# Optimization experiments

Measured on AMD Instinct MI355X. Metric: run time of the kernel, lower is better.

The kernel has to match this reference:

```python
import jax, jax.numpy as jnp
import numpy as np
from jax import lax

B, N, NPOINT, NSAMPLE = 8, 8192, 1024, 32
IN_CH = 64
MLP = [128, 128, 256]
EPS = 1e-5  # BatchNorm eps (inference mode with running stats)


def setup_inputs() -> dict:
    key = jax.random.key(0)
    ks = jax.random.split(key, 2 + len(MLP))
    inp = {
        "xyz": jax.random.normal(ks[0], (B, N, 3), jnp.float32),
        "feature": jax.random.normal(ks[1], (B, IN_CH, N), jnp.float32),
    }
    last = IN_CH
    for li, out in enumerate(MLP):
        k = jax.random.split(ks[2 + li], 3)
        inp[f"w{li}"] = jax.random.normal(k[0], (out, last), jnp.float32) / np.sqrt(last).astype(np.float32)
        inp[f"b{li}"] = jnp.zeros((out,), jnp.float32)
        inp[f"gamma{li}"] = jnp.ones((out,), jnp.float32)
        inp[f"beta{li}"] = jnp.zeros((out,), jnp.float32)
        inp[f"mean{li}"] = 0.1 * jax.random.normal(k[1], (out,), jnp.float32)
        inp[f"var{li}"] = 1.0 + 0.1 * jax.random.uniform(k[2], (out,), jnp.float32)
        last = out
    return inp


def furthest_point_sample(xyz, npoint):
    # xyz: [B, N, 3] -> idx [B, npoint] (sequential FPS via scan)
    Bn, Nn, _ = xyz.shape
    start = jnp.zeros((Bn,), jnp.int32)

    def step(carry, _):
        mind, last = carry
        p = jnp.take_along_axis(xyz, last[:, None, None], axis=1)  # [B,1,3]
        d = jnp.sum((xyz - p) ** 2, axis=-1)  # [B,N]
        mind = jnp.minimum(mind, d)
        nxt = jnp.argmax(mind, axis=-1).astype(jnp.int32)
        return (mind, nxt), nxt

    init = (jnp.full((Bn, Nn), 1e10, xyz.dtype), start)
    _, rest = lax.scan(step, init, None, length=npoint - 1)  # [npoint-1, B]
    return jnp.concatenate([start[None, :], rest], axis=0).T  # [B, npoint]


def k_neighbor_query(new_xyz, xyz, k):
    # squared distances via ||a||^2 + ||b||^2 - 2 a.b  (no [B,S,N,3] blowup)
    d = (jnp.sum(new_xyz ** 2, -1)[:, :, None]
         + jnp.sum(xyz ** 2, -1)[:, None, :]
         - 2.0 * jnp.einsum('bsc,bnc->bsn', new_xyz, xyz))  # [B,S,N]
    _, idx = lax.top_k(-d, k)  # k smallest distances
    return idx  # [B,S,k]


def _mlp_layers(x, params):
    # x: [B, Cin, S, k]; each layer: 1x1 conv -> BN (running stats) -> ReLU
    for (w, b, g, bt, m, v) in params:
        y = jnp.einsum('oi,bisk->bosk', w, x) + b[None, :, None, None]
        inv = (g / jnp.sqrt(v + EPS))[None, :, None, None]
        x = jax.nn.relu((y - m[None, :, None, None]) * inv + bt[None, :, None, None])
    return x


def reference(xyz, feature,
              w0, b0, gamma0, beta0, mean0, var0,
              w1, b1, gamma1, beta1, mean1, var1,
              w2, b2, gamma2, beta2, mean2, var2):
    idx = furthest_point_sample(xyz, NPOINT)                     # [B,S]
    new_xyz = jnp.take_along_axis(xyz, idx[:, :, None], axis=1)  # [B,S,3]
    nidx = k_neighbor_query(new_xyz, xyz, NSAMPLE)               # [B,S,k]
    # grouping_operation: gather neighbor features -> [B,D,S,k]
    grouped = jax.vmap(lambda f, i: f[:, i])(feature, nidx)
    params = [(w0, b0, gamma0, beta0, mean0, var0),
              (w1, b1, gamma1, beta1, mean1, var1),
              (w2, b2, gamma2, beta2, mean2, var2)]
    x = _mlp_layers(grouped, params)
    new_feature = jnp.max(x, axis=3)  # [B, D', S]
    return new_xyz, new_feature
```

## Files before the change

kernel.cpp:

```cpp
#include <hip/hip_runtime.h>
#include <hip/hip_bf16.h>
#include <math.h>

#define B_  8
#define N_  8192
#define S_  1024
#define K_  32
#define C0_ 64
#define NW  248
#define BINS 2048
#define CCAP 256

typedef __attribute__((ext_vector_type(8))) short short8;
typedef __attribute__((ext_vector_type(4))) float f32x4;
typedef __attribute__((ext_vector_type(2))) float f32x2;

#define WH_OFF   0
#define WL_OFF   114688
#define SC_OFF   229376
#define SH_OFF   231424
#define FT_OFF   233472
#define NIDX_OFF 8622080
#define PROG_OFF 9670656
#define WL0E 0
#define WL1E 8192
#define WL2E 24576

__device__ __forceinline__ void split_bf16(float x, unsigned short& h, unsigned short& l) {
    __hip_bfloat16 hb = __float2bfloat16(x);
    float hf = __bfloat162float(hb);
    __hip_bfloat16 lb = __float2bfloat16(x - hf);
    h = *(unsigned short*)&hb;
    l = *(unsigned short*)&lb;
}

__device__ __forceinline__ f32x4 mfma16(short8 a, short8 b, f32x4 c) {
    return __builtin_amdgcn_mfma_f32_16x16x32_bf16(a, b, c, 0, 0, 0);
}

template<int CTRL, int RMASK>
__device__ __forceinline__ unsigned long long dpp_max_step(unsigned long long k) {
    unsigned lo = (unsigned)k, hi = (unsigned)(k >> 32);
    unsigned tlo = (unsigned)__builtin_amdgcn_update_dpp(0, (int)lo, CTRL, RMASK, 0xF, false);
    unsigned thi = (unsigned)__builtin_amdgcn_update_dpp(0, (int)hi, CTRL, RMASK, 0xF, false);
    unsigned long long t = ((unsigned long long)thi << 32) | (unsigned long long)tlo;
    return (t > k) ? t : k;
}
__device__ __forceinline__ unsigned long long wave_max_u64(unsigned long long k) {
    k = dpp_max_step<0x111, 0xF>(k);
    k = dpp_max_step<0x112, 0xF>(k);
    k = dpp_max_step<0x114, 0xF>(k);
    k = dpp_max_step<0x118, 0xF>(k);
    k = dpp_max_step<0x142, 0xA>(k);
    k = dpp_max_step<0x143, 0xC>(k);
    return k;
}
__device__ __forceinline__ unsigned long long umax64(unsigned long long a, unsigned long long b) {
    return (a > b) ? a : b;
}

struct KnnSh {
    unsigned hist[2][BINS];
    unsigned long long cand[2][CCAP];
    unsigned long long kslots[2][2][4];
    int sel[2][K_];
    unsigned wpart[2][4];
    int sBin[2], sBelow[2];
    unsigned cnt_sel[2], cnt_cand[2];
    int fallback;
};

__global__ __launch_bounds__(512) void fused_kernel(
    const float* __restrict__ xyz, const float* __restrict__ feature,
    const float* __restrict__ w0, const float* __restrict__ w1, const float* __restrict__ w2,
    const float* __restrict__ b0, const float* __restrict__ g0, const float* __restrict__ be0,
    const float* __restrict__ m0, const float* __restrict__ v0,
    const float* __restrict__ b1, const float* __restrict__ g1, const float* __restrict__ be1,
    const float* __restrict__ m1, const float* __restrict__ v1,
    const float* __restrict__ b2, const float* __restrict__ g2, const float* __restrict__ be2,
    const float* __restrict__ m2, const float* __restrict__ v2,
    char* __restrict__ ws, float* __restrict__ out)
{
    __shared__ __align__(16) char smraw[131584];
    const int tid = threadIdx.x;
    const int bid = (int)blockIdx.x;

    if (bid < B_) {
        #pragma clang fp contract(off)
        const int b = bid;
        float4* xyzw = (float4*)smraw;
        unsigned long long* wredA = (unsigned long long*)(smraw + N_ * 16);
        unsigned long long* wredB = wredA + 8;
        int* prog = (int*)(ws + PROG_OFF) + b * 16;

        f32x2 px[8], py[8], pz[8], mind[8];
        const float* xb = xyz + (size_t)b * N_ * 3;
        #pragma unroll
        for (int j = 0; j < 8; ++j) {
            int n0 = (2 * j) * 512 + tid, n1 = n0 + 512;
            float x0 = xb[n0 * 3], y0 = xb[n0 * 3 + 1], z0 = xb[n0 * 3 + 2];
            float x1 = xb[n1 * 3], y1 = xb[n1 * 3 + 1], z1 = xb[n1 * 3 + 2];
            px[j] = (f32x2){x0, x1}; py[j] = (f32x2){y0, y1}; pz[j] = (f32x2){z0, z1};
            xyzw[n0] = make_float4(x0, y0, z0, 0.f);
            xyzw[n1] = make_float4(x1, y1, z1, 0.f);
            mind[j] = (f32x2){1e10f, 1e10f};
        }
        __syncthreads();

        float4 p0 = xyzw[0];
        float lx = p0.x, ly = p0.y, lz = p0.z;
        if (tid == 0) {
            float* d0 = out + (size_t)b * S_ * 3;
            d0[0] = lx; d0[1] = ly; d0[2] = lz;
        }
        const int lane = tid & 63, wid = tid >> 6;

        for (int it = 1; it < S_; ++it) {
            f32x2 lx2 = (f32x2){lx, lx}, ly2 = (f32x2){ly, ly}, lz2 = (f32x2){lz, lz};
            float bv = -1.0f; int bj = 0;
            #pragma unroll
            for (int j = 0; j < 8; ++j) {
                f32x2 dx = px[j] - lx2;
                f32x2 dy = py[j] - ly2;
                f32x2 dz = pz[j] - lz2;
                f32x2 t = dx * dx;
                t = t + dy * dy;
                t = t + dz * dz;
                f32x2 mv = mind[j];
                float m0v = fminf(mv.x, t.x);
                float m1v = fminf(mv.y, t.y);
                mind[j] = (f32x2){m0v, m1v};
                if (m0v > bv) { bv = m0v; bj = 2 * j; }
                if (m1v > bv) { bv = m1v; bj = 2 * j + 1; }
            }
            unsigned long long key =
                ((unsigned long long)__float_as_uint(bv) << 32) |
                (unsigned long long)(0xFFFFFFFFu - (unsigned)(bj * 512 + tid));
            key = wave_max_u64(key);
            unsigned long long* wred = (it & 1) ? wredA : wredB;
            if (lane == 63) wred[wid] = key;
            __syncthreads();
            unsigned long long g0v = umax64(wred[0], wred[1]);
            unsigned long long g1v = umax64(wred[2], wred[3]);
            unsigned long long g2v = umax64(wred[4], wred[5]);
            unsigned long long g3v = umax64(wred[6], wred[7]);
            unsigned long long g = umax64(umax64(g0v, g1v), umax64(g2v, g3v));
            int ns = (int)(0xFFFFFFFFu - (unsigned)(g & 0xFFFFFFFFull));
            float4 p = xyzw[ns];
            lx = p.x; ly = p.y; lz = p.z;
            if (tid == 0) {
                float* d0 = out + ((size_t)b * S_ + it) * 3;
                d0[0] = lx; d0[1] = ly; d0[2] = lz;
                if ((it & 7) == 7)
                    __hip_atomic_store(prog, it + 1, __ATOMIC_RELEASE, __HIP_MEMORY_SCOPE_AGENT);
            }
        }
        if (tid == 0)
            __hip_atomic_store(prog, S_, __ATOMIC_RELEASE, __HIP_MEMORY_SCOPE_AGENT);
        return;
    }

    const int w = bid - B_;

    {
        unsigned short* th = (unsigned short*)smraw;
        for (int t = w; t < 1024; t += NW) {
            int bb = t >> 7, n0 = (t & 127) * 64;
            __syncthreads();
            {
                int cg = tid >> 6, ln = tid & 63;
                const float* fb = feature + (size_t)bb * C0_ * N_;
                #pragma unroll
                for (int i = 0; i < 8; ++i) {
                    int c = cg * 8 + i;
                    __hip_bfloat16 hb = __float2bfloat16(fb[(size_t)c * N_ + n0 + ln]);
                    th[ln * 72 + c] = *(unsigned short*)&hb;
                }
            }
            __syncthreads();
            {
                int n = tid >> 3, c0 = (tid & 7) * 8;
                unsigned short* ft = (unsigned short*)(ws + FT_OFF) + ((size_t)(bb * N_ + n0 + n)) * C0_ + c0;
                *(short8*)ft = *(const short8*)(th + n * 72 + c0);
            }
        }
    }
    if (w < 112) {
        int i = w * 512 + tid;
        float x;
        if (i < WL1E)      x = w0[i];
        else if (i < WL2E) x = w1[i - WL1E];
        else               x = w2[i - WL2E];
        unsigned short h, l;
        split_bf16(x, h, l);
        ((unsigned short*)(ws + WH_OFF))[i] = h;
        ((unsigned short*)(ws + WL_OFF))[i] = l;
    } else if (w == 112) {
        int o = tid;
        if (o < 512) {
            const float *bb_, *gg, *be_, *mm, *vv; int oo;
            if (o < 128)      { bb_ = b0; gg = g0; be_ = be0; mm = m0; vv = v0; oo = o; }
            else if (o < 256) { bb_ = b1; gg = g1; be_ = be1; mm = m1; vv = v1; oo = o - 128; }
            else              { bb_ = b2; gg = g2; be_ = be2; mm = m2; vv = v2; oo = o - 256; }
            float scv = gg[oo] / sqrtf(vv[oo] + 1e-5f);
            ((float*)(ws + SC_OFF))[o] = scv;
            ((float*)(ws + SH_OFF))[o] = (bb_[oo] - mm[oo]) * scv + be_[oo];
        }
    }

    KnnSh* S = (KnnSh*)smraw;
    const int ht = tid & 255, half = tid >> 8;
    const int lane = tid & 63, widH = (tid >> 6) & 3;
    int* nidx = (int*)(ws + NIDX_OFF);

    for (int p = 0; p < 17; ++p) {
        int qA = p * (NW * 2) + w * 2;
        int q = qA + half;
        bool active = q < B_ * S_;
        int qc = active ? q : (B_ * S_ - 1);
        int s = qc >> 3, bq = qc & 7;

        if (tid == 0) {
            int qB = qA + 1;
            int needA = (qA < B_ * S_) ? ((qA >> 3) + 1) : 0;
            int needB = (qB < B_ * S_) ? ((qB >> 3) + 1) : 0;
            const int* pga = (const int*)(ws + PROG_OFF) + (qA & 7) * 16;
            const int* pgb = (const int*)(ws + PROG_OFF) + ((qA + 1) & 7) * 16;
            for (;;) {
                int pa = needA ? __hip_atomic_load(pga, __ATOMIC_ACQUIRE, __HIP_MEMORY_SCOPE_AGENT) : 0x7fffffff;
                int pb = needB ? __hip_atomic_load(pgb, __ATOMIC_ACQUIRE, __HIP_MEMORY_SCOPE_AGENT) : 0x7fffffff;
                if (pa >= needA && pb >= needB) break;
                __builtin_amdgcn_s_sleep(8);
            }
        }
        __syncthreads();
        if (active)
            (void)__hip_atomic_load((const int*)(ws + PROG_OFF) + bq * 16,
                                    __ATOMIC_ACQUIRE, __HIP_MEMORY_SCOPE_AGENT);

        #pragma unroll
        for (int i = 0; i < BINS / 256; ++i) S->hist[half][ht + i * 256] = 0;
        if (ht == 0) { S->cnt_sel[half] = 0; S->cnt_cand[half] = 0; if (tid == 0) S->fallback = 0; }

        const float* qp = out + (size_t)(bq * S_ + s) * 3;
        float qx = qp[0], qy = qp[1], qz = qp[2];
        float sa = __fadd_rn(__fadd_rn(__fmul_rn(qx, qx), __fmul_rn(qy, qy)), __fmul_rn(qz, qz));

        unsigned key[32];
        const float* base = xyz + (size_t)bq * N_ * 3;
        #pragma unroll
        for (int i = 0; i < 32; ++i) {
            int n = i * 256 + ht;
            float x = base[n * 3], y = base[n * 3 + 1], z = base[n * 3 + 2];
            float sb  = __fadd_rn(__fadd_rn(__fmul_rn(x, x), __fmul_rn(y, y)), __fmul_rn(z, z));
            float dot = __fadd_rn(__fadd_rn(__fmul_rn(qx, x), __fmul_rn(qy, y)), __fmul_rn(qz, z));
            float d   = __fsub_rn(__fadd_rn(sa, sb), __fmul_rn(2.0f, dot));
            unsigned u = __float_as_uint(d);
            key[i] = u ^ (unsigned)(((int)u >> 31) | (int)0x80000000);
        }
        __syncthreads();
        if (active) {
            #pragma unroll
            for (int i = 0; i < 32; ++i) atomicAdd(&S->hist[half][key[i] >> 21], 1u);
        }
        __syncthreads();

        unsigned h8[8], lsum = 0;
        #pragma unroll
        for (int i = 0; i < 8; ++i) { h8[i] = S->hist[half][ht * 8 + i]; lsum += h8[i]; }
        unsigned inc = lsum;
        #pragma unroll
        for (int off = 1; off < 64; off <<= 1) {
            unsigned o = __shfl_up(inc, off);
            if (lane >= off) inc += o;
        }
        if (lane == 63) S->wpart[half][widH] = inc;
        __syncthreads();
        unsigned basec = 0;
        #pragma unroll
        for (int w4 = 0; w4 < 4; ++w4) if (w4 < widH) basec += S->wpart[half][w4];
        unsigned excl = basec + inc - lsum;
        if (active && excl < (unsigned)K_ && excl + lsum >= (unsigned)K_) {
            unsigned c = excl;
            #pragma unroll
            for (int i = 0; i < 8; ++i) {
                if (c < (unsigned)K_ && c + h8[i] >= (unsigned)K_) { S->sBin[half] = ht * 8 + i; S->sBelow[half] = (int)c; }
                c += h8[i];
            }
        }
        __syncthreads();
        const unsigned Bbin = (unsigned)S->sBin[half];
        const int below = S->sBelow[half];

        if (active) {
            #pragma unroll
            for (int i = 0; i < 32; ++i) {
                unsigned bin = key[i] >> 21;
                int n = i * 256 + ht;
                if (bin < Bbin) {
                    unsigned pp = atomicAdd(&S->cnt_sel[half], 1u);
                    if (pp < (unsigned)K_) S->sel[half][pp] = n;
                } else if (bin == Bbin) {
                    unsigned pp = atomicAdd(&S->cnt_cand[half], 1u);
                    if (pp < CCAP) S->cand[half][pp] = ((unsigned long long)key[i] << 32) | (unsigned)n;
                }
            }
        }
        __syncthreads();
        int m = (int)S->cnt_cand[half];
        if (active && ht == 0 && m > CCAP) S->fallback = 1;
        __syncthreads();

        if (!S->fallback) {
            if (widH == 0) {
                int mtake = active ? (K_ - below) : 0;
                if (mtake < 0) mtake = 0; if (mtake > K_) mtake = K_;
                int mm = active ? m : 0;
                unsigned long long v[4];
                #pragma unroll
                for (int j = 0; j < 4; ++j) {
                    int pp = lane + j * 64;
                    v[j] = (pp < mm) ? S->cand[half][pp] : ~0ull;
                }
                for (int r = 0; r < mtake; ++r) {
                    unsigned long long loc = v[0];
                    #pragma unroll
                    for (int j = 1; j < 4; ++j) if (v[j] < loc) loc = v[j];
                    unsigned long long g = loc;
                    #pragma unroll
                    for (int off = 1; off < 64; off <<= 1) {
                        unsigned long long o = __shfl_xor(g, off);
                        if (o < g) g = o;
                    }
                    #pragma unroll
                    for (int j = 0; j < 4; ++j) if (v[j] == g) v[j] = ~0ull;
                    if (lane == 0) S->sel[half][below + r] = (int)(unsigned)(g & 0xFFFFFFFFull);
                }
            }
            __syncthreads();
        } else {
            unsigned bk = 0xFFFFFFFFu; int bi = 0;
            #pragma unroll
            for (int i = 0; i < 32; ++i) if (key[i] < bk) { bk = key[i]; bi = i; }
            for (int r = 0; r < K_; ++r) {
                unsigned long long pk = ((unsigned long long)bk << 32) | (unsigned)(bi * 256 + ht);
                #pragma unroll
                for (int off = 1; off < 64; off <<= 1) {
                    unsigned long long o = __shfl_xor(pk, off);
                    if (o < pk) pk = o;
                }
                if (lane == 0) S->kslots[half][r & 1][widH] = pk;
                __syncthreads();
                unsigned long long g = S->kslots[half][r & 1][0];
                #pragma unroll
                for (int w4 = 1; w4 < 4; ++w4) { unsigned long long o = S->kslots[half][r & 1][w4]; if (o < g) g = o; }
                int wn = (int)(unsigned)(g & 0xFFFFFFFFull);
                if (ht == 0) S->sel[half][r] = wn;
                if ((wn & 255) == ht) {
                    int iw = wn >> 8;
                    #pragma unroll
                    for (int ii = 0; ii < 32; ++ii) if (ii == iw) key[ii] = 0xFFFFFFFFu;
                    bk = 0xFFFFFFFFu; bi = 0;
                    #pragma unroll
                    for (int ii = 0; ii < 32; ++ii) if (key[ii] < bk) { bk = key[ii]; bi = ii; }
                }
            }
            __syncthreads();
        }
        if (active && ht < K_) nidx[((size_t)(bq * S_ + s)) * K_ + ht] = S->sel[half][ht];
        __syncthreads();
    }
}

template<int AF, int KC, bool LAST>
__device__ __forceinline__ void layer(
    const unsigned short* __restrict__ Xin, int rsi,
    unsigned short* __restrict__ Xout,
    const unsigned short* __restrict__ Wh, const unsigned short* __restrict__ Wl,
    const float* __restrict__ sc, const float* __restrict__ sh,
    float* __restrict__ outg, int wid, int ln15, int quad)
{
    const int K = KC * 32;
    f32x4 acc[AF][8];
    #pragma unroll
    for (int a = 0; a < AF; ++a)
        #pragma unroll
        for (int j = 0; j < 8; ++j) acc[a][j] = (f32x4){0.f, 0.f, 0.f, 0.f};

    #pragma unroll
    for (int kc = 0; kc < KC; ++kc) {
        const int k0 = kc * 32 + quad * 8;
        short8 bf[8];
        #pragma unroll
        for (int j = 0; j < 8; ++j)
            bf[j] = *(const short8*)(Xin + (j * 16 + ln15) * rsi + k0);
        #pragma unroll
        for (int a = 0; a < AF; ++a) {
            const int row = wid * (AF * 16) + a * 16 + ln15;
            short8 ah = *(const short8*)(Wh + (size_t)row * K + k0);
            short8 al = *(const short8*)(Wl + (size_t)row * K + k0);
            #pragma unroll
            for (int j = 0; j < 8; ++j) {
                acc[a][j] = mfma16(al, bf[j], acc[a][j]);
                acc[a][j] = mfma16(ah, bf[j], acc[a][j]);
            }
        }
    }
    #pragma unroll
    for (int a = 0; a < AF; ++a) {
        const int o4 = wid * (AF * 16) + a * 16 + quad * 4;
        f32x4 scv = *(const f32x4*)(sc + o4);
        f32x4 shv = *(const f32x4*)(sh + o4);
        if (LAST) {
            #pragma unroll
            for (int qq = 0; qq < 4; ++qq) {
                float m4[4];
                #pragma unroll
                for (int r = 0; r < 4; ++r) {
                    float v0 = fmaxf(acc[a][2 * qq][r]     * scv[r] + shv[r], 0.f);
                    float v1 = fmaxf(acc[a][2 * qq + 1][r] * scv[r] + shv[r], 0.f);
                    float mm = fmaxf(v0, v1);
                    mm = fmaxf(mm, __shfl_xor(mm, 1));
                    mm = fmaxf(mm, __shfl_xor(mm, 2));
                    mm = fmaxf(mm, __shfl_xor(mm, 4));
                    mm = fmaxf(mm, __shfl_xor(mm, 8));
                    m4[r] = mm;
                }
                if (ln15 == 0) {
                    #pragma unroll
                    for (int r = 0; r < 4; ++r)
                        outg[(size_t)(o4 + r) * S_ + qq] = m4[r];
                }
            }
        } else {
            #pragma unroll
            for (int j = 0; j < 8; ++j) {
                unsigned short pq[4];
                #pragma unroll
                for (int r = 0; r < 4; ++r) {
                    float v = fmaxf(acc[a][j][r] * scv[r] + shv[r], 0.f);
                    __hip_bfloat16 hb = __float2bfloat16(v);
                    pq[r] = *(unsigned short*)&hb;
                }
                *(unsigned long long*)(Xout + (j * 16 + ln15) * 136 + o4) = *(unsigned long long*)pq;
            }
        }
    }
}

__global__ __launch_bounds__(256, 2) void mlp_kernel(
    const char* __restrict__ ws, float* __restrict__ out)
{
    __shared__ __align__(16) unsigned short XA[128 * 136];
    __shared__ __align__(16) unsigned short XB[128 * 136];
    __shared__ int nid[128];

    const int tid = threadIdx.x;
    const int b = blockIdx.x >> 8;
    const int s0 = (blockIdx.x & 255) * 4;
    const int lane = tid & 63, wid = tid >> 6;
    const int ln15 = lane & 15, quad = lane >> 4;

    const int* nidx = (const int*)(ws + NIDX_OFF);
    if (tid < 128) nid[tid] = nidx[((size_t)(b * S_ + s0)) * K_ + tid];
    __syncthreads();

    const unsigned short* FT = (const unsigned short*)(ws + FT_OFF);
    #pragma unroll
    for (int it = 0; it < 4; ++it) {
        int idx = it * 256 + tid;
        int row = idx >> 3, slot = idx & 7;
        short8 v = *(const short8*)(FT + ((size_t)(b * N_ + nid[row])) * C0_ + slot * 8);
        *(short8*)(XA + row * 72 + slot * 8) = v;
    }
    __syncthreads();

    const unsigned short* Wh = (const unsigned short*)(ws + WH_OFF);
    const unsigned short* Wl = (const unsigned short*)(ws + WL_OFF);
    const float* sc = (const float*)(ws + SC_OFF);
    const float* sh = (const float*)(ws + SH_OFF);

    layer<2, 2, false>(XA, 72,  XB, Wh + WL0E, Wl + WL0E, sc,       sh,       nullptr, wid, ln15, quad);
    __syncthreads();
    layer<2, 4, false>(XB, 136, XA, Wh + WL1E, Wl + WL1E, sc + 128, sh + 128, nullptr, wid, ln15, quad);
    __syncthreads();
    float* outg = out + (size_t)B_ * S_ * 3 + (size_t)b * 256 * S_ + s0;
    layer<4, 4, true>(XA, 136, nullptr, Wh + WL2E, Wl + WL2E, sc + 256, sh + 256, outg, wid, ln15, quad);
}

extern "C" void kernel_launch(void* const* d_in, const int* in_sizes, int n_in,
                              void* d_out, int out_size, void* d_ws, size_t ws_size,
                              hipStream_t stream) {
    const float* xyz     = (const float*)d_in[0];
    const float* feature = (const float*)d_in[1];
    const float* w0 = (const float*)d_in[2];
    const float* b0 = (const float*)d_in[3];
    const float* g0 = (const float*)d_in[4];
    const float* be0 = (const float*)d_in[5];
    const float* m0 = (const float*)d_in[6];
    const float* v0 = (const float*)d_in[7];
    const float* w1 = (const float*)d_in[8];
    const float* b1 = (const float*)d_in[9];
    const float* g1 = (const float*)d_in[10];
    const float* be1 = (const float*)d_in[11];
    const float* m1 = (const float*)d_in[12];
    const float* v1 = (const float*)d_in[13];
    const float* w2 = (const float*)d_in[14];
    const float* b2 = (const float*)d_in[15];
    const float* g2 = (const float*)d_in[16];
    const float* be2 = (const float*)d_in[17];
    const float* m2 = (const float*)d_in[18];
    const float* v2 = (const float*)d_in[19];

    float* out = (float*)d_out;
    char*  ws  = (char*)d_ws;

    void* kargs[] = {
        (void*)&xyz, (void*)&feature, (void*)&w0, (void*)&w1, (void*)&w2,
        (void*)&b0, (void*)&g0, (void*)&be0, (void*)&m0, (void*)&v0,
        (void*)&b1, (void*)&g1, (void*)&be1, (void*)&m1, (void*)&v1,
        (void*)&b2, (void*)&g2, (void*)&be2, (void*)&m2, (void*)&v2,
        (void*)&ws, (void*)&out };
    hipError_t ce = hipLaunchCooperativeKernel((void*)fused_kernel,
                                               dim3(B_ + NW), dim3(512), kargs, 0, stream);
    if (ce != hipSuccess) {
        fused_kernel<<<B_ + NW, 512, 0, stream>>>(xyz, feature, w0, w1, w2,
            b0, g0, be0, m0, v0, b1, g1, be1, m1, v1, b2, g2, be2, m2, v2, ws, out);
    }
    mlp_kernel<<<B_ * S_ / 4, 256, 0, stream>>>((const char*)ws, out);
}
```

Measured before the change: 1.420 ms.

## Fuse MLP into persistent cooperative kernel with per-query flag streaming

Folds the separate MLP kernel into the cooperative fused kernel, adding dedicated MLP blocks that spin on tagged neighbor-index entries (query id packed into the high 32 bits) and process query groups as KNN finishes them. FPS publishes per-point slots instead of a coarse progress counter, and KNN blocks are reduced to 184 with a per-block ready flag. The goal is to overlap the MLP with the sequential FPS/KNN tail and remove the second launch. The cost is heavier spin-waiting, a fixed block split that can leave work imbalanced, and a dependence on all blocks being co-resident.

```diff
diff --git a/kernel.cpp b/kernel.cpp
--- a/kernel.cpp
+++ b/kernel.cpp
@@ -7,7 +7,9 @@
 #define S_  1024
 #define K_  32
 #define C0_ 64
-#define NW  248
+#define NK  184
+#define NM  64
+#define NP_KNN 23
 #define BINS 2048
 #define CCAP 256
 
@@ -15,16 +17,18 @@
 typedef __attribute__((ext_vector_type(4))) float f32x4;
 typedef __attribute__((ext_vector_type(2))) float f32x2;
 
-#define WH_OFF   0
-#define WL_OFF   114688
-#define SC_OFF   229376
-#define SH_OFF   231424
-#define FT_OFF   233472
-#define NIDX_OFF 8622080
-#define PROG_OFF 9670656
+#define WH_OFF    0
+#define WL_OFF    114688
+#define SC_OFF    229376
+#define SH_OFF    231424
+#define FT_OFF    233472
+#define NIDX2_OFF 8622080
+#define SLOT_OFF  10719232
+#define FLAG_OFF  10915840
 #define WL0E 0
 #define WL1E 8192
 #define WL2E 24576
+#define FLAG_MAGIC(w) (0x5AB00000u | (unsigned)(w))
 
 __device__ __forceinline__ void split_bf16(float x, unsigned short& h, unsigned short& l) {
     __hip_bfloat16 hb = __float2bfloat16(x);
@@ -57,6 +61,13 @@
 }
 __device__ __forceinline__ unsigned long long umax64(unsigned long long a, unsigned long long b) {
     return (a > b) ? a : b;
+}
+
+__device__ __forceinline__ void block_sync_lds() {
+    asm volatile("" ::: "memory");
+    __builtin_amdgcn_s_waitcnt(0xC07F);
+    __builtin_amdgcn_s_barrier();
+    asm volatile("" ::: "memory");
 }
 
 struct KnnSh {
@@ -68,309 +79,8 @@
     int sBin[2], sBelow[2];
     unsigned cnt_sel[2], cnt_cand[2];
     int fallback;
+    float qpt[2][4];
 };
-
-__global__ __launch_bounds__(512) void fused_kernel(
-    const float* __restrict__ xyz, const float* __restrict__ feature,
-    const float* __restrict__ w0, const float* __restrict__ w1, const float* __restrict__ w2,
-    const float* __restrict__ b0, const float* __restrict__ g0, const float* __restrict__ be0,
-    const float* __restrict__ m0, const float* __restrict__ v0,
-    const float* __restrict__ b1, const float* __restrict__ g1, const float* __restrict__ be1,
-    const float* __restrict__ m1, const float* __restrict__ v1,
-    const float* __restrict__ b2, const float* __restrict__ g2, const float* __restrict__ be2,
-    const float* __restrict__ m2, const float* __restrict__ v2,
-    char* __restrict__ ws, float* __restrict__ out)
-{
-    __shared__ __align__(16) char smraw[131584];
-    const int tid = threadIdx.x;
-    const int bid = (int)blockIdx.x;
-
-    if (bid < B_) {
-        #pragma clang fp contract(off)
-        const int b = bid;
-        float4* xyzw = (float4*)smraw;
-        unsigned long long* wredA = (unsigned long long*)(smraw + N_ * 16);
-        unsigned long long* wredB = wredA + 8;
-        int* prog = (int*)(ws + PROG_OFF) + b * 16;
-
-        f32x2 px[8], py[8], pz[8], mind[8];
-        const float* xb = xyz + (size_t)b * N_ * 3;
-        #pragma unroll
-        for (int j = 0; j < 8; ++j) {
-            int n0 = (2 * j) * 512 + tid, n1 = n0 + 512;
-            float x0 = xb[n0 * 3], y0 = xb[n0 * 3 + 1], z0 = xb[n0 * 3 + 2];
-            float x1 = xb[n1 * 3], y1 = xb[n1 * 3 + 1], z1 = xb[n1 * 3 + 2];
-            px[j] = (f32x2){x0, x1}; py[j] = (f32x2){y0, y1}; pz[j] = (f32x2){z0, z1};
-            xyzw[n0] = make_float4(x0, y0, z0, 0.f);
-            xyzw[n1] = make_float4(x1, y1, z1, 0.f);
-            mind[j] = (f32x2){1e10f, 1e10f};
-        }
-        __syncthreads();
-
-        float4 p0 = xyzw[0];
-        float lx = p0.x, ly = p0.y, lz = p0.z;
-        if (tid == 0) {
-            float* d0 = out + (size_t)b * S_ * 3;
-            d0[0] = lx; d0[1] = ly; d0[2] = lz;
-        }
-        const int lane = tid & 63, wid = tid >> 6;
-
-        for (int it = 1; it < S_; ++it) {
-            f32x2 lx2 = (f32x2){lx, lx}, ly2 = (f32x2){ly, ly}, lz2 = (f32x2){lz, lz};
-            float bv = -1.0f; int bj = 0;
-            #pragma unroll
-            for (int j = 0; j < 8; ++j) {
-                f32x2 dx = px[j] - lx2;
-                f32x2 dy = py[j] - ly2;
-                f32x2 dz = pz[j] - lz2;
-                f32x2 t = dx * dx;
-                t = t + dy * dy;
-                t = t + dz * dz;
-                f32x2 mv = mind[j];
-                float m0v = fminf(mv.x, t.x);
-                float m1v = fminf(mv.y, t.y);
-                mind[j] = (f32x2){m0v, m1v};
-                if (m0v > bv) { bv = m0v; bj = 2 * j; }
-                if (m1v > bv) { bv = m1v; bj = 2 * j + 1; }
-            }
-            unsigned long long key =
-                ((unsigned long long)__float_as_uint(bv) << 32) |
-                (unsigned long long)(0xFFFFFFFFu - (unsigned)(bj * 512 + tid));
-            key = wave_max_u64(key);
-            unsigned long long* wred = (it & 1) ? wredA : wredB;
-            if (lane == 63) wred[wid] = key;
-            __syncthreads();
-            unsigned long long g0v = umax64(wred[0], wred[1]);
-            unsigned long long g1v = umax64(wred[2], wred[3]);
-            unsigned long long g2v = umax64(wred[4], wred[5]);
-            unsigned long long g3v = umax64(wred[6], wred[7]);
-            unsigned long long g = umax64(umax64(g0v, g1v), umax64(g2v, g3v));
-            int ns = (int)(0xFFFFFFFFu - (unsigned)(g & 0xFFFFFFFFull));
-            float4 p = xyzw[ns];
-            lx = p.x; ly = p.y; lz = p.z;
-            if (tid == 0) {
-                float* d0 = out + ((size_t)b * S_ + it) * 3;
-                d0[0] = lx; d0[1] = ly; d0[2] = lz;
-                if ((it & 7) == 7)
-                    __hip_atomic_store(prog, it + 1, __ATOMIC_RELEASE, __HIP_MEMORY_SCOPE_AGENT);
-            }
-        }
-        if (tid == 0)
-            __hip_atomic_store(prog, S_, __ATOMIC_RELEASE, __HIP_MEMORY_SCOPE_AGENT);
-        return;
-    }
-
-    const int w = bid - B_;
-
-    {
-        unsigned short* th = (unsigned short*)smraw;
-        for (int t = w; t < 1024; t += NW) {
-            int bb = t >> 7, n0 = (t & 127) * 64;
-            __syncthreads();
-            {
-                int cg = tid >> 6, ln = tid & 63;
-                const float* fb = feature + (size_t)bb * C0_ * N_;
-                #pragma unroll
-                for (int i = 0; i < 8; ++i) {
-                    int c = cg * 8 + i;
-                    __hip_bfloat16 hb = __float2bfloat16(fb[(size_t)c * N_ + n0 + ln]);
-                    th[ln * 72 + c] = *(unsigned short*)&hb;
-                }
-            }
-            __syncthreads();
-            {
-                int n = tid >> 3, c0 = (tid & 7) * 8;
-                unsigned short* ft = (unsigned short*)(ws + FT_OFF) + ((size_t)(bb * N_ + n0 + n)) * C0_ + c0;
-                *(short8*)ft = *(const short8*)(th + n * 72 + c0);
-            }
-        }
-    }
-    if (w < 112) {
-        int i = w * 512 + tid;
-        float x;
-        if (i < WL1E)      x = w0[i];
-        else if (i < WL2E) x = w1[i - WL1E];
-        else               x = w2[i - WL2E];
-        unsigned short h, l;
-        split_bf16(x, h, l);
-        ((unsigned short*)(ws + WH_OFF))[i] = h;
-        ((unsigned short*)(ws + WL_OFF))[i] = l;
-    } else if (w == 112) {
-        int o = tid;
-        if (o < 512) {
-            const float *bb_, *gg, *be_, *mm, *vv; int oo;
-            if (o < 128)      { bb_ = b0; gg = g0; be_ = be0; mm = m0; vv = v0; oo = o; }
-            else if (o < 256) { bb_ = b1; gg = g1; be_ = be1; mm = m1; vv = v1; oo = o - 128; }
-            else              { bb_ = b2; gg = g2; be_ = be2; mm = m2; vv = v2; oo = o - 256; }
-            float scv = gg[oo] / sqrtf(vv[oo] + 1e-5f);
-            ((float*)(ws + SC_OFF))[o] = scv;
-            ((float*)(ws + SH_OFF))[o] = (bb_[oo] - mm[oo]) * scv + be_[oo];
-        }
-    }
-
-    KnnSh* S = (KnnSh*)smraw;
-    const int ht = tid & 255, half = tid >> 8;
-    const int lane = tid & 63, widH = (tid >> 6) & 3;
-    int* nidx = (int*)(ws + NIDX_OFF);
-
-    for (int p = 0; p < 17; ++p) {
-        int qA = p * (NW * 2) + w * 2;
-        int q = qA + half;
-        bool active = q < B_ * S_;
-        int qc = active ? q : (B_ * S_ - 1);
-        int s = qc >> 3, bq = qc & 7;
-
-        if (tid == 0) {
-            int qB = qA + 1;
-            int needA = (qA < B_ * S_) ? ((qA >> 3) + 1) : 0;
-            int needB = (qB < B_ * S_) ? ((qB >> 3) + 1) : 0;
-            const int* pga = (const int*)(ws + PROG_OFF) + (qA & 7) * 16;
-            const int* pgb = (const int*)(ws + PROG_OFF) + ((qA + 1) & 7) * 16;
-            for (;;) {
-                int pa = needA ? __hip_atomic_load(pga, __ATOMIC_ACQUIRE, __HIP_MEMORY_SCOPE_AGENT) : 0x7fffffff;
-                int pb = needB ? __hip_atomic_load(pgb, __ATOMIC_ACQUIRE, __HIP_MEMORY_SCOPE_AGENT) : 0x7fffffff;
-                if (pa >= needA && pb >= needB) break;
-                __builtin_amdgcn_s_sleep(8);
-            }
-        }
-        __syncthreads();
-        if (active)
-            (void)__hip_atomic_load((const int*)(ws + PROG_OFF) + bq * 16,
-                                    __ATOMIC_ACQUIRE, __HIP_MEMORY_SCOPE_AGENT);
-
-        #pragma unroll
-        for (int i = 0; i < BINS / 256; ++i) S->hist[half][ht + i * 256] = 0;
-        if (ht == 0) { S->cnt_sel[half] = 0; S->cnt_cand[half] = 0; if (tid == 0) S->fallback = 0; }
-
-        const float* qp = out + (size_t)(bq * S_ + s) * 3;
-        float qx = qp[0], qy = qp[1], qz = qp[2];
-        float sa = __fadd_rn(__fadd_rn(__fmul_rn(qx, qx), __fmul_rn(qy, qy)), __fmul_rn(qz, qz));
-
-        unsigned key[32];
-        const float* base = xyz + (size_t)bq * N_ * 3;
-        #pragma unroll
-        for (int i = 0; i < 32; ++i) {
-            int n = i * 256 + ht;
-            float x = base[n * 3], y = base[n * 3 + 1], z = base[n * 3 + 2];
-            float sb  = __fadd_rn(__fadd_rn(__fmul_rn(x, x), __fmul_rn(y, y)), __fmul_rn(z, z));
-            float dot = __fadd_rn(__fadd_rn(__fmul_rn(qx, x), __fmul_rn(qy, y)), __fmul_rn(qz, z));
-            float d   = __fsub_rn(__fadd_rn(sa, sb), __fmul_rn(2.0f, dot));
-            unsigned u = __float_as_uint(d);
-            key[i] = u ^ (unsigned)(((int)u >> 31) | (int)0x80000000);
-        }
-        __syncthreads();
-        if (active) {
-            #pragma unroll
-            for (int i = 0; i < 32; ++i) atomicAdd(&S->hist[half][key[i] >> 21], 1u);
-        }
-        __syncthreads();
-
-        unsigned h8[8], lsum = 0;
-        #pragma unroll
-        for (int i = 0; i < 8; ++i) { h8[i] = S->hist[half][ht * 8 + i]; lsum += h8[i]; }
-        unsigned inc = lsum;
-        #pragma unroll
-        for (int off = 1; off < 64; off <<= 1) {
-            unsigned o = __shfl_up(inc, off);
-            if (lane >= off) inc += o;
-        }
-        if (lane == 63) S->wpart[half][widH] = inc;
-        __syncthreads();
-        unsigned basec = 0;
-        #pragma unroll
-        for (int w4 = 0; w4 < 4; ++w4) if (w4 < widH) basec += S->wpart[half][w4];
-        unsigned excl = basec + inc - lsum;
-        if (active && excl < (unsigned)K_ && excl + lsum >= (unsigned)K_) {
-            unsigned c = excl;
-            #pragma unroll
-            for (int i = 0; i < 8; ++i) {
-                if (c < (unsigned)K_ && c + h8[i] >= (unsigned)K_) { S->sBin[half] = ht * 8 + i; S->sBelow[half] = (int)c; }
-                c += h8[i];
-            }
-        }
-        __syncthreads();
-        const unsigned Bbin = (unsigned)S->sBin[half];
-        const int below = S->sBelow[half];
-
-        if (active) {
-            #pragma unroll
-            for (int i = 0; i < 32; ++i) {
-                unsigned bin = key[i] >> 21;
-                int n = i * 256 + ht;
-                if (bin < Bbin) {
-                    unsigned pp = atomicAdd(&S->cnt_sel[half], 1u);
-                    if (pp < (unsigned)K_) S->sel[half][pp] = n;
-                } else if (bin == Bbin) {
-                    unsigned pp = atomicAdd(&S->cnt_cand[half], 1u);
-                    if (pp < CCAP) S->cand[half][pp] = ((unsigned long long)key[i] << 32) | (unsigned)n;
-                }
-            }
-        }
-        __syncthreads();
-        int m = (int)S->cnt_cand[half];
-        if (active && ht == 0 && m > CCAP) S->fallback = 1;
-        __syncthreads();
-
-        if (!S->fallback) {
-            if (widH == 0) {
-                int mtake = active ? (K_ - below) : 0;
-                if (mtake < 0) mtake = 0; if (mtake > K_) mtake = K_;
-                int mm = active ? m : 0;
-                unsigned long long v[4];
-                #pragma unroll
-                for (int j = 0; j < 4; ++j) {
-                    int pp = lane + j * 64;
-                    v[j] = (pp < mm) ? S->cand[half][pp] : ~0ull;
-                }
-                for (int r = 0; r < mtake; ++r) {
-                    unsigned long long loc = v[0];
-                    #pragma unroll
-                    for (int j = 1; j < 4; ++j) if (v[j] < loc) loc = v[j];
-                    unsigned long long g = loc;
-                    #pragma unroll
-                    for (int off = 1; off < 64; off <<= 1) {
-                        unsigned long long o = __shfl_xor(g, off);
-                        if (o < g) g = o;
-                    }
-                    #pragma unroll
-                    for (int j = 0; j < 4; ++j) if (v[j] == g) v[j] = ~0ull;
-                    if (lane == 0) S->sel[half][below + r] = (int)(unsigned)(g & 0xFFFFFFFFull);
-                }
-            }
-            __syncthreads();
-        } else {
-            unsigned bk = 0xFFFFFFFFu; int bi = 0;
-            #pragma unroll
-            for (int i = 0; i < 32; ++i) if (key[i] < bk) { bk = key[i]; bi = i; }
-            for (int r = 0; r < K_; ++r) {
-                unsigned long long pk = ((unsigned long long)bk << 32) | (unsigned)(bi * 256 + ht);
-                #pragma unroll
-                for (int off = 1; off < 64; off <<= 1) {
-                    unsigned long long o = __shfl_xor(pk, off);
-                    if (o < pk) pk = o;
-                }
-                if (lane == 0) S->kslots[half][r & 1][widH] = pk;
-                __syncthreads();
-                unsigned long long g = S->kslots[half][r & 1][0];
-                #pragma unroll
-                for (int w4 = 1; w4 < 4; ++w4) { unsigned long long o = S->kslots[half][r & 1][w4]; if (o < g) g = o; }
-                int wn = (int)(unsigned)(g & 0xFFFFFFFFull);
-                if (ht == 0) S->sel[half][r] = wn;
-                if ((wn & 255) == ht) {
-                    int iw = wn >> 8;
-                    #pragma unroll
-                    for (int ii = 0; ii < 32; ++ii) if (ii == iw) key[ii] = 0xFFFFFFFFu;
-                    bk = 0xFFFFFFFFu; bi = 0;
-                    #pragma unroll
-                    for (int ii = 0; ii < 32; ++ii) if (key[ii] < bk) { bk = key[ii]; bi = ii; }
-                }
-            }
-            __syncthreads();
-        }
-        if (active && ht < K_) nidx[((size_t)(bq * S_ + s)) * K_ + ht] = S->sel[half][ht];
-        __syncthreads();
-    }
-}
 
 template<int AF, int KC, bool LAST>
 __device__ __forceinline__ void layer(
@@ -448,44 +158,385 @@
     }
 }
 
-__global__ __launch_bounds__(256, 2) void mlp_kernel(
-    const char* __restrict__ ws, float* __restrict__ out)
+__global__ __launch_bounds__(512, 2) void fused_kernel(
+    const float* __restrict__ xyz, const float* __restrict__ feature,
+    const float* __restrict__ w0, const float* __restrict__ w1, const float* __restrict__ w2,
+    const float* __restrict__ b0, const float* __restrict__ g0, const float* __restrict__ be0,
+    const float* __restrict__ m0, const float* __restrict__ v0,
+    const float* __restrict__ b1, const float* __restrict__ g1, const float* __restrict__ be1,
+    const float* __restrict__ m1, const float* __restrict__ v1,
+    const float* __restrict__ b2, const float* __restrict__ g2, const float* __restrict__ be2,
+    const float* __restrict__ m2, const float* __restrict__ v2,
+    char* __restrict__ ws, float* __restrict__ out)
 {
-    __shared__ __align__(16) unsigned short XA[128 * 136];
-    __shared__ __align__(16) unsigned short XB[128 * 136];
-    __shared__ int nid[128];
-
+    __shared__ __align__(16) char smraw[131584];
     const int tid = threadIdx.x;
-    const int b = blockIdx.x >> 8;
-    const int s0 = (blockIdx.x & 255) * 4;
-    const int lane = tid & 63, wid = tid >> 6;
-    const int ln15 = lane & 15, quad = lane >> 4;
-
-    const int* nidx = (const int*)(ws + NIDX_OFF);
-    if (tid < 128) nid[tid] = nidx[((size_t)(b * S_ + s0)) * K_ + tid];
-    __syncthreads();
-
-    const unsigned short* FT = (const unsigned short*)(ws + FT_OFF);
-    #pragma unroll
-    for (int it = 0; it < 4; ++it) {
-        int idx = it * 256 + tid;
-        int row = idx >> 3, slot = idx & 7;
-        short8 v = *(const short8*)(FT + ((size_t)(b * N_ + nid[row])) * C0_ + slot * 8);
-        *(short8*)(XA + row * 72 + slot * 8) = v;
+    const int bid = (int)blockIdx.x;
+
+    if (bid < B_) {
+        #pragma clang fp contract(off)
+        const int b = bid;
+        float4* xyzw = (float4*)smraw;
+        unsigned long long* wredA = (unsigned long long*)(smraw + N_ * 16);
+        unsigned long long* wredB = wredA + 8;
+        unsigned long long* slots = (unsigned long long*)(ws + SLOT_OFF) + (size_t)b * S_ * 3;
+
+        f32x2 px[8], py[8], pz[8], mind[8];
+        const float* xb = xyz + (size_t)b * N_ * 3;
+        #pragma unroll
+        for (int j = 0; j < 8; ++j) {
+            int n0 = (2 * j) * 512 + tid, n1 = n0 + 512;
+            float x0 = xb[n0 * 3], y0 = xb[n0 * 3 + 1], z0 = xb[n0 * 3 + 2];
+            float x1 = xb[n1 * 3], y1 = xb[n1 * 3 + 1], z1 = xb[n1 * 3 + 2];
+            px[j] = (f32x2){x0, x1}; py[j] = (f32x2){y0, y1}; pz[j] = (f32x2){z0, z1};
+            xyzw[n0] = make_float4(x0, y0, z0, 0.f);
+            xyzw[n1] = make_float4(x1, y1, z1, 0.f);
+            mind[j] = (f32x2){1e10f, 1e10f};
+        }
+        __syncthreads();
+
+        float4 p0 = xyzw[0];
+        float lx = p0.x, ly = p0.y, lz = p0.z;
+        if (tid < 3) {
+            float v = (tid == 0) ? lx : ((tid == 1) ? ly : lz);
+            __hip_atomic_store(slots + tid, (unsigned long long)__float_as_uint(v),
+                               __ATOMIC_RELAXED, __HIP_MEMORY_SCOPE_AGENT);
+        }
+        const int lane = tid & 63, wid = tid >> 6;
+
+        for (int it = 1; it < S_; ++it) {
+            f32x2 lx2 = (f32x2){lx, lx}, ly2 = (f32x2){ly, ly}, lz2 = (f32x2){lz, lz};
+            float bv = -1.0f; int bj = 0;
+            #pragma unroll
+            for (int j = 0; j < 8; ++j) {
+                f32x2 dx = px[j] - lx2;
+                f32x2 dy = py[j] - ly2;
+                f32x2 dz = pz[j] - lz2;
+                f32x2 t = dx * dx;
+                t = t + dy * dy;
+                t = t + dz * dz;
+                f32x2 mv = mind[j];
+                float m0v = fminf(mv.x, t.x);
+                float m1v = fminf(mv.y, t.y);
+                mind[j] = (f32x2){m0v, m1v};
+                if (m0v > bv) { bv = m0v; bj = 2 * j; }
+                if (m1v > bv) { bv = m1v; bj = 2 * j + 1; }
+            }
+            unsigned long long key =
+                ((unsigned long long)__float_as_uint(bv) << 32) |
+                (unsigned long long)(0xFFFFFFFFu - (unsigned)(bj * 512 + tid));
+            key = wave_max_u64(key);
+            unsigned long long* wred = (it & 1) ? wredA : wredB;
+            if (lane == 63) wred[wid] = key;
+            block_sync_lds();
+            unsigned long long g0v = umax64(wred[0], wred[1]);
+            unsigned long long g1v = umax64(wred[2], wred[3]);
+            unsigned long long g2v = umax64(wred[4], wred[5]);
+            unsigned long long g3v = umax64(wred[6], wred[7]);
+            unsigned long long g = umax64(umax64(g0v, g1v), umax64(g2v, g3v));
+            int ns = (int)(0xFFFFFFFFu - (unsigned)(g & 0xFFFFFFFFull));
+            float4 p = xyzw[ns];
+            lx = p.x; ly = p.y; lz = p.z;
+            if (tid < 3) {
+                float v = (tid == 0) ? lx : ((tid == 1) ? ly : lz);
+                __hip_atomic_store(slots + (size_t)it * 3 + tid,
+                                   (((unsigned long long)(unsigned)it) << 32) | __float_as_uint(v),
+                                   __ATOMIC_RELAXED, __HIP_MEMORY_SCOPE_AGENT);
+            }
+        }
+        return;
     }
-    __syncthreads();
-
-    const unsigned short* Wh = (const unsigned short*)(ws + WH_OFF);
-    const unsigned short* Wl = (const unsigned short*)(ws + WL_OFF);
-    const float* sc = (const float*)(ws + SC_OFF);
-    const float* sh = (const float*)(ws + SH_OFF);
-
-    layer<2, 2, false>(XA, 72,  XB, Wh + WL0E, Wl + WL0E, sc,       sh,       nullptr, wid, ln15, quad);
-    __syncthreads();
-    layer<2, 4, false>(XB, 136, XA, Wh + WL1E, Wl + WL1E, sc + 128, sh + 128, nullptr, wid, ln15, quad);
-    __syncthreads();
-    float* outg = out + (size_t)B_ * S_ * 3 + (size_t)b * 256 * S_ + s0;
-    layer<4, 4, true>(XA, 136, nullptr, Wh + WL2E, Wl + WL2E, sc + 256, sh + 256, outg, wid, ln15, quad);
+
+    if (bid < B_ + NK) {
+        const int w = bid - B_;
+
+        {
+            unsigned short* th = (unsigned short*)smraw;
+            for (int t = w; t < 1024; t += NK) {
+                int bb = t >> 7, n0 = (t & 127) * 64;
+                __syncthreads();
+                {
+                    int cg = tid >> 6, ln = tid & 63;
+                    const float* fb = feature + (size_t)bb * C0_ * N_;
+                    #pragma unroll
+                    for (int i = 0; i < 8; ++i) {
+                        int c = cg * 8 + i;
+                        __hip_bfloat16 hb = __float2bfloat16(fb[(size_t)c * N_ + n0 + ln]);
+                        th[ln * 72 + c] = *(unsigned short*)&hb;
+                    }
+                }
+                __syncthreads();
+                {
+                    int n = tid >> 3, c0 = (tid & 7) * 8;
+                    unsigned short* ft = (unsigned short*)(ws + FT_OFF) + ((size_t)(bb * N_ + n0 + n)) * C0_ + c0;
+                    *(short8*)ft = *(const short8*)(th + n * 72 + c0);
+                }
+            }
+        }
+        if (w < 112) {
+            int i = w * 512 + tid;
+            float x;
+            if (i < WL1E)      x = w0[i];
+            else if (i < WL2E) x = w1[i - WL1E];
+            else               x = w2[i - WL2E];
+            unsigned short h, l;
+            split_bf16(x, h, l);
+            ((unsigned short*)(ws + WH_OFF))[i] = h;
+            ((unsigned short*)(ws + WL_OFF))[i] = l;
+        } else if (w == 112) {
+            int o = tid;
+            if (o < 512) {
+                const float *bb_, *gg, *be_, *mm, *vv; int oo;
+                if (o < 128)      { bb_ = b0; gg = g0; be_ = be0; mm = m0; vv = v0; oo = o; }
+                else if (o < 256) { bb_ = b1; gg = g1; be_ = be1; mm = m1; vv = v1; oo = o - 128; }
+                else              { bb_ = b2; gg = g2; be_ = be2; mm = m2; vv = v2; oo = o - 256; }
+                float scv = gg[oo] / sqrtf(vv[oo] + 1e-5f);
+                ((float*)(ws + SC_OFF))[o] = scv;
+                ((float*)(ws + SH_OFF))[o] = (bb_[oo] - mm[oo]) * scv + be_[oo];
+            }
+        }
+        __syncthreads();
+        if (tid == 0)
+            __hip_atomic_store((unsigned*)(ws + FLAG_OFF) + w, FLAG_MAGIC(w),
+                               __ATOMIC_RELEASE, __HIP_MEMORY_SCOPE_AGENT);
+
+        KnnSh* S = (KnnSh*)smraw;
+        const int ht = tid & 255, half = tid >> 8;
+        const int lane = tid & 63, widH = (tid >> 6) & 3;
+        unsigned long long* nidx2 = (unsigned long long*)(ws + NIDX2_OFF);
+        const unsigned long long* slots = (const unsigned long long*)(ws + SLOT_OFF);
+
+        for (int p = 0; p < NP_KNN; ++p) {
+            int qA = p * (NK * 2) + w * 2;
+            int q = qA + half;
+            bool active = q < B_ * S_;
+            int qc = active ? q : (B_ * S_ - 1);
+            int s = qc >> 3, bq = qc & 7;
+
+            if (tid == 0) {
+                #pragma unroll
+                for (int h = 0; h < 2; ++h) {
+                    int qq = qA + h;
+                    if (qq >= B_ * S_) continue;
+                    int ss = qq >> 3, bb = qq & 7;
+                    const unsigned long long* sl = slots + ((size_t)bb * S_ + ss) * 3;
+                    #pragma unroll
+                    for (int c = 0; c < 3; ++c) {
+                        unsigned long long v;
+                        for (;;) {
+                            v = __hip_atomic_load(sl + c, __ATOMIC_RELAXED, __HIP_MEMORY_SCOPE_AGENT);
+                            if ((int)(v >> 32) == ss) break;
+                            __builtin_amdgcn_s_sleep(8);
+                        }
+                        S->qpt[h][c] = __uint_as_float((unsigned)v);
+                    }
+                }
+            }
+            __syncthreads();
+
+            if (active && ht < 3) out[(size_t)(bq * S_ + s) * 3 + ht] = S->qpt[half][ht];
+
+            #pragma unroll
+            for (int i = 0; i < BINS / 256; ++i) S->hist[half][ht + i * 256] = 0;
+            if (ht == 0) { S->cnt_sel[half] = 0; S->cnt_cand[half] = 0; if (tid == 0) S->fallback = 0; }
+
+            float qx = S->qpt[half][0], qy = S->qpt[half][1], qz = S->qpt[half][2];
+            float sa = __fadd_rn(__fadd_rn(__fmul_rn(qx, qx), __fmul_rn(qy, qy)), __fmul_rn(qz, qz));
+
+            unsigned key[32];
+            const float* base = xyz + (size_t)bq * N_ * 3;
+            #pragma unroll
+            for (int i = 0; i < 32; ++i) {
+                int n = i * 256 + ht;
+                float x = base[n * 3], y = base[n * 3 + 1], z = base[n * 3 + 2];
+                float sb  = __fadd_rn(__fadd_rn(__fmul_rn(x, x), __fmul_rn(y, y)), __fmul_rn(z, z));
+                float dot = __fadd_rn(__fadd_rn(__fmul_rn(qx, x), __fmul_rn(qy, y)), __fmul_rn(qz, z));
+                float d   = __fsub_rn(__fadd_rn(sa, sb), __fmul_rn(2.0f, dot));
+                unsigned u = __float_as_uint(d);
+                key[i] = u ^ (unsigned)(((int)u >> 31) | (int)0x80000000);
+            }
+            __syncthreads();
+            if (active) {
+                #pragma unroll
+                for (int i = 0; i < 32; ++i) atomicAdd(&S->hist[half][key[i] >> 21], 1u);
+            }
+            __syncthreads();
+
+            unsigned h8[8], lsum = 0;
+            #pragma unroll
+            for (int i = 0; i < 8; ++i) { h8[i] = S->hist[half][ht * 8 + i]; lsum += h8[i]; }
+            unsigned inc = lsum;
+            #pragma unroll
+            for (int off = 1; off < 64; off <<= 1) {
+                unsigned o = __shfl_up(inc, off);
+                if (lane >= off) inc += o;
+            }
+            if (lane == 63) S->wpart[half][widH] = inc;
+            __syncthreads();
+            unsigned basec = 0;
+            #pragma unroll
+            for (int w4 = 0; w4 < 4; ++w4) if (w4 < widH) basec += S->wpart[half][w4];
+            unsigned excl = basec + inc - lsum;
+            if (active && excl < (unsigned)K_ && excl + lsum >= (unsigned)K_) {
+                unsigned c = excl;
+                #pragma unroll
+                for (int i = 0; i < 8; ++i) {
+                    if (c < (unsigned)K_ && c + h8[i] >= (unsigned)K_) { S->sBin[half] = ht * 8 + i; S->sBelow[half] = (int)c; }
+                    c += h8[i];
+                }
+            }
+            __syncthreads();
+            const unsigned Bbin = (unsigned)S->sBin[half];
+            const int below = S->sBelow[half];
+
+            if (active) {
+                #pragma unroll
+                for (int i = 0; i < 32; ++i) {
+                    unsigned bin = key[i] >> 21;
+                    int n = i * 256 + ht;
+                    if (bin < Bbin) {
+                        unsigned pp = atomicAdd(&S->cnt_sel[half], 1u);
+                        if (pp < (unsigned)K_) S->sel[half][pp] = n;
+                    } else if (bin == Bbin) {
+                        unsigned pp = atomicAdd(&S->cnt_cand[half], 1u);
+                        if (pp < CCAP) S->cand[half][pp] = ((unsigned long long)key[i] << 32) | (unsigned)n;
+                    }
+                }
+            }
+            __syncthreads();
+            int m = (int)S->cnt_cand[half];
+            if (active && ht == 0 && m > CCAP) S->fallback = 1;
+            __syncthreads();
+
+            if (!S->fallback) {
+                if (widH == 0) {
+                    int mtake = active ? (K_ - below) : 0;
+                    if (mtake < 0) mtake = 0; if (mtake > K_) mtake = K_;
+                    int mm = active ? m : 0;
+                    unsigned long long v[4];
+                    #pragma unroll
+                    for (int j = 0; j < 4; ++j) {
+                        int pp = lane + j * 64;
+                        v[j] = (pp < mm) ? S->cand[half][pp] : ~0ull;
+                    }
+                    for (int r = 0; r < mtake; ++r) {
+                        unsigned long long loc = v[0];
+                        #pragma unroll
+                        for (int j = 1; j < 4; ++j) if (v[j] < loc) loc = v[j];
+                        unsigned long long g = loc;
+                        #pragma unroll
+                        for (int off = 1; off < 64; off <<= 1) {
+                            unsigned long long o = __shfl_xor(g, off);
+                            if (o < g) g = o;
+                        }
+                        #pragma unroll
+                        for (int j = 0; j < 4; ++j) if (v[j] == g) v[j] = ~0ull;
+                        if (lane == 0) S->sel[half][below + r] = (int)(unsigned)(g & 0xFFFFFFFFull);
+                    }
+                }
+                __syncthreads();
+            } else {
+                unsigned bk = 0xFFFFFFFFu; int bi = 0;
+                #pragma unroll
+                for (int i = 0; i < 32; ++i) if (key[i] < bk) { bk = key[i]; bi = i; }
+                for (int r = 0; r < K_; ++r) {
+                    unsigned long long pk = ((unsigned long long)bk << 32) | (unsigned)(bi * 256 + ht);
+                    #pragma unroll
+                    for (int off = 1; off < 64; off <<= 1) {
+                        unsigned long long o = __shfl_xor(pk, off);
+                        if (o < pk) pk = o;
+                    }
+                    if (lane == 0) S->kslots[half][r & 1][widH] = pk;
+                    __syncthreads();
+                    unsigned long long g = S->kslots[half][r & 1][0];
+                    #pragma unroll
+                    for (int w4 = 1; w4 < 4; ++w4) { unsigned long long o = S->kslots[half][r & 1][w4]; if (o < g) g = o; }
+                    int wn = (int)(unsigned)(g & 0xFFFFFFFFull);
+                    if (ht == 0) S->sel[half][r] = wn;
+                    if ((wn & 255) == ht) {
+                        int iw = wn >> 8;
+                        #pragma unroll
+                        for (int ii = 0; ii < 32; ++ii) if (ii == iw) key[ii] = 0xFFFFFFFFu;
+                        bk = 0xFFFFFFFFu; bi = 0;
+                        #pragma unroll
+                        for (int ii = 0; ii < 32; ++ii) if (key[ii] < bk) { bk = key[ii]; bi = ii; }
+                    }
+                }
+                __syncthreads();
+            }
+            if (active && ht < K_)
+                __hip_atomic_store(nidx2 + (size_t)q * K_ + ht,
+                                   (((unsigned long long)(unsigned)q) << 32) | (unsigned)S->sel[half][ht],
+                                   __ATOMIC_RELAXED, __HIP_MEMORY_SCOPE_AGENT);
+            __syncthreads();
+        }
+        return;
+    }
+
+    {
+        const int m = bid - B_ - NK;
+        const int ht = tid & 255;
+        const int lane = tid & 63, widH = (tid >> 6) & 3;
+        const int ln15 = lane & 15, quad = lane >> 4;
+
+        unsigned short* XA = (unsigned short*)smraw;
+        unsigned short* XB = (unsigned short*)(smraw + 34816);
+        int* nid = (int*)(smraw + 69632);
+
+        {
+            volatile unsigned* fl = (volatile unsigned*)(ws + FLAG_OFF);
+            if (tid < NK) {
+                while (__hip_atomic_load((const unsigned*)(ws + FLAG_OFF) + tid,
+                                         __ATOMIC_RELAXED, __HIP_MEMORY_SCOPE_AGENT) != FLAG_MAGIC(tid))
+                    __builtin_amdgcn_s_sleep(16);
+            }
+            (void)fl;
+            __syncthreads();
+            if (tid == 0) __threadfence();
+            __syncthreads();
+        }
+
+        const unsigned short* FT = (const unsigned short*)(ws + FT_OFF);
+        const unsigned short* Wh = (const unsigned short*)(ws + WH_OFF);
+        const unsigned short* Wl = (const unsigned short*)(ws + WL_OFF);
+        const float* sc = (const float*)(ws + SC_OFF);
+        const float* sh = (const float*)(ws + SH_OFF);
+        const unsigned long long* nidx2 = (const unsigned long long*)(ws + NIDX2_OFF);
+
+        for (int t = m; t < 2048; t += NM) {
+            int s4 = t >> 3, bq = t & 7, s0 = s4 * 4;
+            if (ht < 128) {
+                int qi = ht >> 5, k = ht & 31;
+                int q = bq + 8 * (s0 + qi);
+                const unsigned long long* ptr = nidx2 + (size_t)q * K_ + k;
+                unsigned long long v;
+                for (;;) {
+                    v = __hip_atomic_load(ptr, __ATOMIC_RELAXED, __HIP_MEMORY_SCOPE_AGENT);
+                    if ((int)(v >> 32) == q) break;
+                    __builtin_amdgcn_s_sleep(8);
+                }
+                nid[ht] = (int)(unsigned)(v & 0xFFFFFFFFull);
+            }
+            __syncthreads();
+
+            #pragma unroll
+            for (int it = 0; it < 4; ++it) {
+                int idx = it * 256 + ht;
+                int row = idx >> 3, slot = idx & 7;
+                short8 v = *(const short8*)(FT + ((size_t)(bq * N_ + nid[row])) * C0_ + slot * 8);
+                *(short8*)(XA + row * 72 + slot * 8) = v;
+            }
+            __syncthreads();
+
+            layer<2, 2, false>(XA, 72,  XB, Wh + WL0E, Wl + WL0E, sc,       sh,       nullptr, widH, ln15, quad);
+            __syncthreads();
+            layer<2, 4, false>(XB, 136, XA, Wh + WL1E, Wl + WL1E, sc + 128, sh + 128, nullptr, widH, ln15, quad);
+            __syncthreads();
+            float* outg = out + (size_t)B_ * S_ * 3 + (size_t)bq * 256 * S_ + s0;
+            layer<4, 4, true>(XA, 136, nullptr, Wh + WL2E, Wl + WL2E, sc + 256, sh + 256, outg, widH, ln15, quad);
+            __syncthreads();
+        }
+    }
 }
 
 extern "C" void kernel_launch(void* const* d_in, const int* in_sizes, int n_in,
@@ -522,10 +573,9 @@
         (void*)&b2, (void*)&g2, (void*)&be2, (void*)&m2, (void*)&v2,
         (void*)&ws, (void*)&out };
     hipError_t ce = hipLaunchCooperativeKernel((void*)fused_kernel,
-                                               dim3(B_ + NW), dim3(512), kargs, 0, stream);
+                                               dim3(B_ + NK + NM), dim3(512), kargs, 0, stream);
     if (ce != hipSuccess) {
-        fused_kernel<<<B_ + NW, 512, 0, stream>>>(xyz, feature, w0, w1, w2,
+        fused_kernel<<<B_ + NK + NM, 512, 0, stream>>>(xyz, feature, w0, w1, w2,
             b0, g0, be0, m0, v0, b1, g1, be1, m1, v1, b2, g2, be2, m2, v2, ws, out);
     }
-    mlp_kernel<<<B_ * S_ / 4, 256, 0, stream>>>((const char*)ws, out);
-}
+}
```

Result: faster. 1.256 ms (-11.5%).
